# Optimization experiments

Hardware: AMD Instinct MI355X
Metric: run time of the kernel (lower is better)

## Reference

```python
import jax, jax.numpy as jnp
import numpy as np

B, TQ, TK = 2, 2048, 2048
D_IN, D_OUT, H = 1024, 1024, 16
HD = D_OUT // H  # head dim = 64


def setup_inputs() -> dict:
    key = jax.random.key(0)
    ks = jax.random.split(key, 11)
    s = 1.0 / np.sqrt(D_IN)
    so = 1.0 / np.sqrt(D_OUT)
    return {
        "q": jax.random.normal(ks[0], (B, TQ, D_IN), jnp.float32),
        "k": jax.random.normal(ks[1], (B, TK, D_IN), jnp.float32),
        "v": jax.random.normal(ks[2], (B, TK, D_IN), jnp.float32),
        "Wq": jax.random.uniform(ks[3], (D_OUT, D_IN), jnp.float32, -s, s),
        "bq": jax.random.uniform(ks[4], (D_OUT,), jnp.float32, -s, s),
        "Wk": jax.random.uniform(ks[5], (D_OUT, D_IN), jnp.float32, -s, s),
        "bk": jax.random.uniform(ks[6], (D_OUT,), jnp.float32, -s, s),
        "Wv": jax.random.uniform(ks[7], (D_OUT, D_IN), jnp.float32, -s, s),
        "bv": jax.random.uniform(ks[8], (D_OUT,), jnp.float32, -s, s),
        "Wo": jax.random.uniform(ks[9], (D_OUT, D_OUT), jnp.float32, -so, so),
        "bo": jax.random.uniform(ks[10], (D_OUT,), jnp.float32, -so, so),
    }


def reference(q, k, v, Wq, bq, Wk, bk, Wv, bv, Wo, bo):
    b, tq, _ = q.shape
    tk = k.shape[1]
    # linear projections, split heads: [B,T,D] -> [B,H,T,HD]
    qh = (q @ Wq.T + bq).reshape(b, tq, H, HD).transpose(0, 2, 1, 3)
    kh = (k @ Wk.T + bk).reshape(b, tk, H, HD).transpose(0, 2, 1, 3)
    vh = (v @ Wv.T + bv).reshape(b, tk, H, HD).transpose(0, 2, 1, 3)
    # scaled dot-product attention (forward never applies the causal mask)
    scores = jnp.einsum("bhqd,bhkd->bhqk", qh, kh) / np.sqrt(HD).astype(np.float32)
    attn = jax.nn.softmax(scores, axis=-1)
    x = jnp.einsum("bhqk,bhkd->bhqd", attn, vh)
    x = x.transpose(0, 2, 1, 3).reshape(b, tq, D_OUT)
    return x @ Wo.T + bo
```

## Files before the change

### kernel.cpp

```cpp
#include <hip/hip_runtime.h>
#include <hip/hip_bf16.h>

typedef __bf16 b16x8 __attribute__((ext_vector_type(8)));
typedef unsigned short u16x8 __attribute__((ext_vector_type(8)));
typedef unsigned short u16x4 __attribute__((ext_vector_type(4)));
typedef unsigned int u32x4 __attribute__((ext_vector_type(4)));
typedef unsigned int u32x2 __attribute__((ext_vector_type(2)));
typedef float f32x4 __attribute__((ext_vector_type(4)));
typedef float f32x16 __attribute__((ext_vector_type(16)));

__device__ __forceinline__ unsigned short f2b(float f) {
  unsigned u = __builtin_bit_cast(unsigned, f);
  u += 0x7fff + ((u >> 16) & 1);
  return (unsigned short)(u >> 16);
}

__device__ __forceinline__ b16x8 as_b(u16x8 v) { return __builtin_bit_cast(b16x8, v); }

__device__ __forceinline__ float fexp2(float x) {
#if __has_builtin(__builtin_amdgcn_exp2f)
  return __builtin_amdgcn_exp2f(x);
#else
  return exp2f(x);
#endif
}

__device__ __forceinline__ unsigned cvtpk(float lo, float hi) {
  unsigned r;
  asm("v_cvt_pk_bf16_f32 %0, %1, %2" : "=v"(r) : "v"(lo), "v"(hi));
  return r;
}

__device__ __forceinline__ void plswap(unsigned& a, unsigned& b) {
  asm volatile("v_permlane32_swap_b32 %0, %1" : "+v"(a), "+v"(b));
}

__device__ __forceinline__ b16x8 mkchunk(float p0, float p1, float p2, float p3,
                                         float p4, float p5, float p6, float p7) {
  unsigned a1 = cvtpk(p0, p1), b1 = cvtpk(p4, p5);
  unsigned a2 = cvtpk(p2, p3), b2 = cvtpk(p6, p7);
  plswap(a1, b1);
  plswap(a2, b2);
  u32x4 w = {a1, a2, b1, b2};
  return __builtin_bit_cast(b16x8, w);
}

#define AS1 __attribute__((address_space(1)))
#define AS3 __attribute__((address_space(3)))
__device__ __forceinline__ void gload_lds16(const void* g, void* l) {
  __builtin_amdgcn_global_load_lds((const AS1 void*)g, (AS3 void*)l, 16, 0, 0);
}

#define WAITV4() asm volatile("s_waitcnt vmcnt(4)" ::: "memory")
#define WAITV0() asm volatile("s_waitcnt vmcnt(0)" ::: "memory")
#define LGKM0()  asm volatile("s_waitcnt lgkmcnt(0)" ::: "memory")
#define BARRIER() asm volatile("s_barrier" ::: "memory")


__global__ __launch_bounds__(256) void convert_kernel(
    const float* __restrict__ q, const float* __restrict__ k, const float* __restrict__ v,
    const float* __restrict__ Wq, const float* __restrict__ Wk,
    const float* __restrict__ Wv, const float* __restrict__ Wo,
    unsigned short* __restrict__ qb, unsigned short* __restrict__ kb,
    unsigned short* __restrict__ vb, unsigned short* __restrict__ wqb,
    unsigned short* __restrict__ wkb, unsigned short* __restrict__ wvb,
    unsigned short* __restrict__ wob) {
  const float* src; unsigned short* dst; int rows;
  switch (blockIdx.y) {
    case 0: src = q;  dst = qb;  rows = 4096; break;
    case 1: src = k;  dst = kb;  rows = 4096; break;
    case 2: src = v;  dst = vb;  rows = 4096; break;
    case 3: src = Wq; dst = wqb; rows = 1024; break;
    case 4: src = Wk; dst = wkb; rows = 1024; break;
    case 5: src = Wv; dst = wvb; rows = 1024; break;
    default: src = Wo; dst = wob; rows = 1024; break;
  }
  const int row = blockIdx.x * 2 + (threadIdx.x >> 7);
  if (row >= rows) return;
  const int t = threadIdx.x & 127;
  const float* sp = src + (size_t)row * 1024 + t * 8;
  float4 f0 = *(const float4*)sp;
  float4 f1 = *(const float4*)(sp + 4);
  u16x8 h = { f2b(f0.x), f2b(f0.y), f2b(f0.z), f2b(f0.w),
              f2b(f1.x), f2b(f1.y), f2b(f1.z), f2b(f1.w) };
  const int swcol = ((t >> 3) << 6) | (((t & 7) ^ (row & 7)) << 3);
  *(u16x8*)(dst + (size_t)row * 1024 + swcol) = h;
}

template <int MODE, typename TOUT>
__device__ __forceinline__ void gemm_compute_step(const unsigned short* sA,
                                                  const unsigned short* sB,
                                                  f32x4 (&acc)[2][4],
                                                  int wm, int wn, int lr, int lg) {
  b16x8 af[2][2], bf[4][2];
#pragma unroll
  for (int mb = 0; mb < 2; ++mb)
#pragma unroll
    for (int kh = 0; kh < 2; ++kh) {
      const int r = wm * 32 + mb * 16 + lr;
      af[mb][kh] = as_b(*(const u16x8*)(&sA[(r * 64 + kh * 32 + lg * 8) ^ ((r & 7) << 3)]));
    }
#pragma unroll
  for (int nb = 0; nb < 4; ++nb)
#pragma unroll
    for (int kh = 0; kh < 2; ++kh) {
      const int r = wn * 64 + nb * 16 + lr;
      bf[nb][kh] = as_b(*(const u16x8*)(&sB[(r * 64 + kh * 32 + lg * 8) ^ ((r & 7) << 3)]));
    }
#pragma unroll
  for (int mb = 0; mb < 2; ++mb)
#pragma unroll
    for (int nb = 0; nb < 4; ++nb) {
      acc[mb][nb] = __builtin_amdgcn_mfma_f32_16x16x32_bf16(af[mb][0], bf[nb][0], acc[mb][nb], 0, 0, 0);
      acc[mb][nb] = __builtin_amdgcn_mfma_f32_16x16x32_bf16(af[mb][1], bf[nb][1], acc[mb][nb], 0, 0, 0);
    }
}

template <int MODE, typename TOUT>
__device__ __forceinline__ void gemm_epilogue(f32x4 (&acc)[2][4],
                                              const float* __restrict__ bias,
                                              TOUT* __restrict__ C,
                                              int bm, int bn, int wm, int wn,
                                              int lr, int lg) {
  const float qscale = 0.125f * 1.44269504f;
#pragma unroll
  for (int mb = 0; mb < 2; ++mb)
#pragma unroll
    for (int nb = 0; nb < 4; ++nb) {
      const int c = bn + wn * 64 + nb * 16 + lr;
      const float bv = bias[c];
      const int r0 = bm + wm * 32 + mb * 16 + lg * 4;
      if constexpr (MODE == 2) {
        const int hh = c >> 6, hd = c & 63;
        const int bb = r0 >> 11, t0 = r0 & 2047;
        u16x4 pk = { f2b(acc[mb][nb][0] + bv), f2b(acc[mb][nb][1] + bv),
                     f2b(acc[mb][nb][2] + bv), f2b(acc[mb][nb][3] + bv) };
        const int tsw = (t0 & ~63) | (((((t0 >> 3) & 7) ^ (hd & 7)) << 3)) | (t0 & 7);
        *(u16x4*)(&C[(((size_t)bb * 16 + hh) * 64 + hd) * 2048 + tsw]) = pk;
      } else {
#pragma unroll
        for (int i = 0; i < 4; ++i) {
          float val = acc[mb][nb][i] + bv;
          if constexpr (MODE == 1) val *= qscale;
          if constexpr (MODE == 3) {
            C[(size_t)(r0 + i) * 1024 + c] = val;
          } else {
            const int cc = (c & ~63) | (((((c >> 3) & 7) ^ ((r0 + i) & 7)) << 3)) | (c & 7);
            C[(size_t)(r0 + i) * 1024 + cc] = (TOUT)f2b(val);
          }
        }
      }
    }
}

template <int MODE, typename TOUT>
__device__ __forceinline__ void gemm_b16A(unsigned short* sA, unsigned short* sB,
                                          const unsigned short* __restrict__ A,
                                          const unsigned short* __restrict__ Bm,
                                          const float* __restrict__ bias,
                                          TOUT* __restrict__ C,
                                          int bm, int bn) {
  const int tid = threadIdx.x;
  const int l = tid & 63, w = tid >> 6;
  const int wm = w >> 1, wn = w & 1;
  const int lr = l & 15, lg = l >> 4;
  const int r8 = l >> 3, sl = l & 7;

  f32x4 acc[2][4] = {};

  for (int k0 = 0; k0 < 1024; k0 += 64) {
#pragma unroll
    for (int i = 0; i < 2; ++i) {
      gload_lds16(A + (size_t)(bm + i * 32 + w * 8 + r8) * 1024 + k0 + sl * 8,
                  &sA[i * 2048 + w * 512]);
    }
#pragma unroll
    for (int i = 0; i < 4; ++i) {
      const int row = i * 32 + w * 8 + r8;
      gload_lds16(Bm + (size_t)(bn + row) * 1024 + k0 + sl * 8, &sB[i * 2048 + w * 512]);
    }
    __syncthreads();
    gemm_compute_step<MODE, TOUT>(sA, sB, acc, wm, wn, lr, lg);
    __syncthreads();
  }
  gemm_epilogue<MODE, TOUT>(acc, bias, C, bm, bn, wm, wn, lr, lg);
}

__global__ __launch_bounds__(256) void proj_kernel(
    const unsigned short* __restrict__ qb, const unsigned short* __restrict__ kb,
    const unsigned short* __restrict__ vb,
    const unsigned short* __restrict__ wqb, const float* __restrict__ bq,
    const unsigned short* __restrict__ wkb, const float* __restrict__ bk,
    const unsigned short* __restrict__ wvb, const float* __restrict__ bv,
    unsigned short* __restrict__ Qh, unsigned short* __restrict__ Kh,
    unsigned short* __restrict__ Vt) {
  __shared__ __align__(16) unsigned short sA[64 * 64];
  __shared__ __align__(16) unsigned short sB[128 * 64];
  const int id = blockIdx.x;
  const int g = id >> 6, r = id & 63;
  const int bn = (r >> 3) * 128;
  const int panel = g * 8 + (r & 7);
  const int bz = panel >> 6;
  const int bm = (panel & 63) * 64;
  if (bz == 0)      gemm_b16A<1, unsigned short>(sA, sB, qb, wqb, bq, Qh, bm, bn);
  else if (bz == 1) gemm_b16A<0, unsigned short>(sA, sB, kb, wkb, bk, Kh, bm, bn);
  else              gemm_b16A<2, unsigned short>(sA, sB, vb, wvb, bv, Vt, bm, bn);
}

__global__ __launch_bounds__(256) void out_kernel(
    const unsigned short* __restrict__ X, const unsigned short* __restrict__ wob,
    const float* __restrict__ bo, float* __restrict__ out) {
  __shared__ __align__(16) unsigned short sA[64 * 64];
  __shared__ __align__(16) unsigned short sB[128 * 64];
  const int id = blockIdx.x;
  const int g = id >> 6, r = id & 63;
  const int bn = (r >> 3) * 128;
  const int bm = (g * 8 + (r & 7)) * 64;
  gemm_b16A<3, float>(sA, sB, X, wob, bo, out, bm, bn);
}

__global__ __launch_bounds__(512, 4) void attn_kernel(
    const unsigned short* __restrict__ Qh, const unsigned short* __restrict__ Kh,
    const unsigned short* __restrict__ Vt, unsigned short* __restrict__ X) {
  __shared__ __align__(16) unsigned short sMem[8][4096];

  const int tid = threadIdx.x;
  const int l = tid & 63, wq = tid >> 6;
  const int half = wq >> 2, w4 = wq & 3;
  const int lq = l & 31, lg = l >> 5;

  const int id = blockIdx.x + (int)(gridDim.x * blockIdx.y);
  const int id2 = (id & 7) * 64 + (id >> 3);
  const int bx = id2 & 15, by = id2 >> 4;
  const int b = by >> 4, h = by & 15;
  const int q0 = bx * 128 + w4 * 32;
  const int kvbase = half * 1024;

  const size_t baseQK = (size_t)b * 2048 * 1024 + (size_t)h * 64;
  const size_t baseV  = ((size_t)(b * 16 + h)) * 64 * 2048;

  unsigned short* sK0 = &sMem[half * 4 + 0][0];
  unsigned short* sK1 = &sMem[half * 4 + 1][0];
  unsigned short* sV0 = &sMem[half * 4 + 2][0];
  unsigned short* sV1 = &sMem[half * 4 + 3][0];

  const int rk = lq & 7;
  b16x8 qf0, qf1, qf2, qf3;
  {
    const unsigned short* qp = Qh + baseQK + (size_t)(q0 + lq) * 1024;
    qf0 = as_b(*(const u16x8*)(qp + (((0 + lg) ^ rk) << 3)));
    qf1 = as_b(*(const u16x8*)(qp + (((2 + lg) ^ rk) << 3)));
    qf2 = as_b(*(const u16x8*)(qp + (((4 + lg) ^ rk) << 3)));
    qf3 = as_b(*(const u16x8*)(qp + (((6 + lg) ^ rk) << 3)));
  }

  const int r8 = l >> 3, sl = l & 7;

  auto stageKV = [&](unsigned short* dK, unsigned short* dV, int kv0) {
#pragma unroll
    for (int i = 0; i < 2; ++i) {
      const int rowb = 16 * w4 + 8 * i;
      gload_lds16(Kh + baseQK + (size_t)(kv0 + rowb + r8) * 1024 + sl * 8, dK + rowb * 64);
      gload_lds16(Vt + baseV + (size_t)(rowb + r8) * 2048 + kv0 + sl * 8, dV + rowb * 64);
    }
  };

  float m_run = 0.f, l_run = 0.f;
  f32x16 Oa = {}, Ob = {};
  const int sw = (lq & 7) << 3;

  auto body = [&](const unsigned short* K_, const unsigned short* V_) {
    f32x16 s0, s1;
#pragma unroll
    for (int j = 0; j < 16; ++j) { s0[j] = -m_run; s1[j] = -m_run; }
    __builtin_amdgcn_s_setprio(1);
#pragma unroll
    for (int c = 0; c < 4; ++c) {
      const int hd8 = c * 16 + 8 * lg;
      b16x8 kf0 = as_b(*(const u16x8*)(&K_[lq * 64 + (hd8 ^ sw)]));
      b16x8 kf1 = as_b(*(const u16x8*)(&K_[(32 + lq) * 64 + (hd8 ^ sw)]));
      b16x8 qf = (c == 0) ? qf0 : (c == 1) ? qf1 : (c == 2) ? qf2 : qf3;
      s0 = __builtin_amdgcn_mfma_f32_32x32x16_bf16(kf0, qf, s0, 0, 0, 0);
      s1 = __builtin_amdgcn_mfma_f32_32x32x16_bf16(kf1, qf, s1, 0, 0, 0);
    }
    __builtin_amdgcn_s_setprio(0);

    float a0 = fmaxf(fmaxf(s0[0], s0[1]), fmaxf(s0[2], s0[3]));
    float a1 = fmaxf(fmaxf(s0[4], s0[5]), fmaxf(s0[6], s0[7]));
    float a2 = fmaxf(fmaxf(s0[8], s0[9]), fmaxf(s0[10], s0[11]));
    float a3 = fmaxf(fmaxf(s0[12], s0[13]), fmaxf(s0[14], s0[15]));
    float a4 = fmaxf(fmaxf(s1[0], s1[1]), fmaxf(s1[2], s1[3]));
    float a5 = fmaxf(fmaxf(s1[4], s1[5]), fmaxf(s1[6], s1[7]));
    float a6 = fmaxf(fmaxf(s1[8], s1[9]), fmaxf(s1[10], s1[11]));
    float a7 = fmaxf(fmaxf(s1[12], s1[13]), fmaxf(s1[14], s1[15]));
    float mx = fmaxf(fmaxf(fmaxf(a0, a1), fmaxf(a2, a3)),
                     fmaxf(fmaxf(a4, a5), fmaxf(a6, a7)));
    mx = fmaxf(mx, __shfl_xor(mx, 32));

    if (__any(mx > 8.0f)) {
      const float dm = fmaxf(mx, 0.f);
      const float al = fexp2(-dm);
      m_run += dm;
      l_run *= al;
#pragma unroll
      for (int j = 0; j < 16; ++j) {
        Oa[j] *= al; Ob[j] *= al; s0[j] -= dm; s1[j] -= dm;
      }
    }

#pragma unroll
    for (int j = 0; j < 16; ++j) s0[j] = fexp2(s0[j]);
#pragma unroll
    for (int j = 0; j < 16; ++j) s1[j] = fexp2(s1[j]);

    float r0 = ((s0[0] + s0[1]) + (s0[2] + s0[3])) + ((s0[4] + s0[5]) + (s0[6] + s0[7]));
    float r1 = ((s0[8] + s0[9]) + (s0[10] + s0[11])) + ((s0[12] + s0[13]) + (s0[14] + s0[15]));
    float r2 = ((s1[0] + s1[1]) + (s1[2] + s1[3])) + ((s1[4] + s1[5]) + (s1[6] + s1[7]));
    float r3 = ((s1[8] + s1[9]) + (s1[10] + s1[11])) + ((s1[12] + s1[13]) + (s1[14] + s1[15]));
    float rs = (r0 + r1) + (r2 + r3);
    rs += __shfl_xor(rs, 32);
    l_run += rs;

    b16x8 pb0 = mkchunk(s0[0], s0[1], s0[2], s0[3], s0[4], s0[5], s0[6], s0[7]);
    b16x8 pb1 = mkchunk(s0[8], s0[9], s0[10], s0[11], s0[12], s0[13], s0[14], s0[15]);
    b16x8 pb2 = mkchunk(s1[0], s1[1], s1[2], s1[3], s1[4], s1[5], s1[6], s1[7]);
    b16x8 pb3 = mkchunk(s1[8], s1[9], s1[10], s1[11], s1[12], s1[13], s1[14], s1[15]);

    __builtin_amdgcn_s_setprio(1);
#pragma unroll
    for (int c = 0; c < 4; ++c) {
      const int kv8 = c * 16 + 8 * lg;
      b16x8 vfa = as_b(*(const u16x8*)(&V_[lq * 64 + (kv8 ^ sw)]));
      b16x8 vfb = as_b(*(const u16x8*)(&V_[(32 + lq) * 64 + (kv8 ^ sw)]));
      b16x8 pb = (c == 0) ? pb0 : (c == 1) ? pb1 : (c == 2) ? pb2 : pb3;
      Oa = __builtin_amdgcn_mfma_f32_32x32x16_bf16(vfa, pb, Oa, 0, 0, 0);
      Ob = __builtin_amdgcn_mfma_f32_32x32x16_bf16(vfb, pb, Ob, 0, 0, 0);
    }
    __builtin_amdgcn_s_setprio(0);
  };

  stageKV(sK0, sV0, kvbase);
  stageKV(sK1, sV1, kvbase + 64);

#pragma unroll 1
  for (int tt = 0; tt < 16; tt += 2) {
    WAITV4();
    BARRIER();
    body(sK0, sV0);
    LGKM0();
    BARRIER();
    if (tt + 2 < 16) stageKV(sK0, sV0, kvbase + (tt + 2) * 64);

    if (tt + 3 < 16) { WAITV4(); } else { WAITV0(); }
    BARRIER();
    body(sK1, sV1);
    LGKM0();
    BARRIER();
    if (tt + 3 < 16) stageKV(sK1, sV1, kvbase + (tt + 3) * 64);
  }

  float* fb = (float*)&sMem[0][0];
  const int mbase = w4 * 64 + l;
  if (half == 1) {
    fb[0 * 256 + mbase] = m_run;
    fb[1 * 256 + mbase] = l_run;
#pragma unroll
    for (int j = 0; j < 16; ++j) fb[(2 + j) * 256 + mbase] = Oa[j];
#pragma unroll
    for (int j = 0; j < 16; ++j) fb[(18 + j) * 256 + mbase] = Ob[j];
  }
  __syncthreads();
  if (half == 0) {
    const float m2 = fb[0 * 256 + mbase], l2 = fb[1 * 256 + mbase];
    const float mM = fmaxf(m_run, m2);
    const float c1 = fexp2(m_run - mM), c2 = fexp2(m2 - mM);
    const float inv = 1.0f / (l_run * c1 + l2 * c2);
    const float ia = c1 * inv, ib = c2 * inv;
#pragma unroll
    for (int j = 0; j < 16; ++j) {
      Oa[j] = Oa[j] * ia + fb[(2 + j) * 256 + mbase] * ib;
      Ob[j] = Ob[j] * ia + fb[(18 + j) * 256 + mbase] * ib;
    }
    unsigned short* xp = X + baseQK + (size_t)(q0 + lq) * 1024;
#pragma unroll
    for (int g = 0; g < 4; ++g) {
      u32x2 wa = { cvtpk(Oa[4 * g + 0], Oa[4 * g + 1]),
                   cvtpk(Oa[4 * g + 2], Oa[4 * g + 3]) };
      *(u32x2*)(xp + ((g ^ rk) << 3) + 4 * lg) = wa;
      u32x2 wb = { cvtpk(Ob[4 * g + 0], Ob[4 * g + 1]),
                   cvtpk(Ob[4 * g + 2], Ob[4 * g + 3]) };
      *(u32x2*)(xp + (((4 + g) ^ rk) << 3) + 4 * lg) = wb;
    }
  }
}

extern "C" void kernel_launch(void* const* d_in, const int* in_sizes, int n_in,
                              void* d_out, int out_size, void* d_ws, size_t ws_size,
                              hipStream_t stream) {
  const float* q  = (const float*)d_in[0];
  const float* k  = (const float*)d_in[1];
  const float* v  = (const float*)d_in[2];
  const float* Wq = (const float*)d_in[3];
  const float* bq = (const float*)d_in[4];
  const float* Wk = (const float*)d_in[5];
  const float* bk = (const float*)d_in[6];
  const float* Wv = (const float*)d_in[7];
  const float* bv = (const float*)d_in[8];
  const float* Wo = (const float*)d_in[9];
  const float* bo = (const float*)d_in[10];

  unsigned short* ws = (unsigned short*)d_ws;
  const size_t M1 = (size_t)1024 * 1024;
  unsigned short* qb  = ws;
  unsigned short* kb  = ws + 4 * M1;
  unsigned short* vb  = ws + 8 * M1;
  unsigned short* wqb = ws + 12 * M1;
  unsigned short* wkb = ws + 13 * M1;
  unsigned short* wvb = ws + 14 * M1;
  unsigned short* wob = ws + 15 * M1;
  unsigned short* Qh  = ws + 16 * M1;
  unsigned short* Kh  = ws + 20 * M1;
  unsigned short* Vt  = ws + 24 * M1;
  unsigned short* X   = qb;

  dim3 blk(256);
  convert_kernel<<<dim3(2048, 7), blk, 0, stream>>>(q, k, v, Wq, Wk, Wv, Wo,
                                                    qb, kb, vb, wqb, wkb, wvb, wob);
  proj_kernel<<<dim3(1536), blk, 0, stream>>>(qb, kb, vb, wqb, bq, wkb, bk, wvb, bv,
                                              Qh, Kh, Vt);
  attn_kernel<<<dim3(16, 32), dim3(512), 0, stream>>>(Qh, Kh, Vt, X);
  out_kernel<<<dim3(512), blk, 0, stream>>>(X, wob, bo, (float*)d_out);
}
```

Before: 117.9 us.

## Single-buffer attention K/V tiles to halve LDS and raise occupancy

The attention kernel drops its double-buffered K/V staging in favour of a single LDS buffer per half, so each iteration loads, waits for all loads, computes and then synchronises. LDS use shrinks and launch bounds go from 4 to 8 blocks per CU, aiming to hide memory latency through more resident waves rather than software prefetch. The GEMM compute step is also inlined directly into the loop. The cost is no overlap of the next tile's loads with the current tile's compute inside a block, plus a tighter register budget that could cause spills.

```diff
diff --git a/kernel.cpp b/kernel.cpp
--- a/kernel.cpp
+++ b/kernel.cpp
@@ -51,9 +51,7 @@
   __builtin_amdgcn_global_load_lds((const AS1 void*)g, (AS3 void*)l, 16, 0, 0);
 }
 
-#define WAITV4() asm volatile("s_waitcnt vmcnt(4)" ::: "memory")
 #define WAITV0() asm volatile("s_waitcnt vmcnt(0)" ::: "memory")
-#define LGKM0()  asm volatile("s_waitcnt lgkmcnt(0)" ::: "memory")
 #define BARRIER() asm volatile("s_barrier" ::: "memory")
 
 
@@ -88,35 +86,6 @@
 }
 
 template <int MODE, typename TOUT>
-__device__ __forceinline__ void gemm_compute_step(const unsigned short* sA,
-                                                  const unsigned short* sB,
-                                                  f32x4 (&acc)[2][4],
-                                                  int wm, int wn, int lr, int lg) {
-  b16x8 af[2][2], bf[4][2];
-#pragma unroll
-  for (int mb = 0; mb < 2; ++mb)
-#pragma unroll
-    for (int kh = 0; kh < 2; ++kh) {
-      const int r = wm * 32 + mb * 16 + lr;
-      af[mb][kh] = as_b(*(const u16x8*)(&sA[(r * 64 + kh * 32 + lg * 8) ^ ((r & 7) << 3)]));
-    }
-#pragma unroll
-  for (int nb = 0; nb < 4; ++nb)
-#pragma unroll
-    for (int kh = 0; kh < 2; ++kh) {
-      const int r = wn * 64 + nb * 16 + lr;
-      bf[nb][kh] = as_b(*(const u16x8*)(&sB[(r * 64 + kh * 32 + lg * 8) ^ ((r & 7) << 3)]));
-    }
-#pragma unroll
-  for (int mb = 0; mb < 2; ++mb)
-#pragma unroll
-    for (int nb = 0; nb < 4; ++nb) {
-      acc[mb][nb] = __builtin_amdgcn_mfma_f32_16x16x32_bf16(af[mb][0], bf[nb][0], acc[mb][nb], 0, 0, 0);
-      acc[mb][nb] = __builtin_amdgcn_mfma_f32_16x16x32_bf16(af[mb][1], bf[nb][1], acc[mb][nb], 0, 0, 0);
-    }
-}
-
-template <int MODE, typename TOUT>
 __device__ __forceinline__ void gemm_epilogue(f32x4 (&acc)[2][4],
                                               const float* __restrict__ bias,
                                               TOUT* __restrict__ C,
@@ -180,7 +149,29 @@
       gload_lds16(Bm + (size_t)(bn + row) * 1024 + k0 + sl * 8, &sB[i * 2048 + w * 512]);
     }
     __syncthreads();
-    gemm_compute_step<MODE, TOUT>(sA, sB, acc, wm, wn, lr, lg);
+
+    b16x8 af[2][2], bf[4][2];
+#pragma unroll
+    for (int mb = 0; mb < 2; ++mb)
+#pragma unroll
+      for (int kh = 0; kh < 2; ++kh) {
+        const int r = wm * 32 + mb * 16 + lr;
+        af[mb][kh] = as_b(*(const u16x8*)(&sA[(r * 64 + kh * 32 + lg * 8) ^ ((r & 7) << 3)]));
+      }
+#pragma unroll
+    for (int nb = 0; nb < 4; ++nb)
+#pragma unroll
+      for (int kh = 0; kh < 2; ++kh) {
+        const int r = wn * 64 + nb * 16 + lr;
+        bf[nb][kh] = as_b(*(const u16x8*)(&sB[(r * 64 + kh * 32 + lg * 8) ^ ((r & 7) << 3)]));
+      }
+#pragma unroll
+    for (int mb = 0; mb < 2; ++mb)
+#pragma unroll
+      for (int nb = 0; nb < 4; ++nb) {
+        acc[mb][nb] = __builtin_amdgcn_mfma_f32_16x16x32_bf16(af[mb][0], bf[nb][0], acc[mb][nb], 0, 0, 0);
+        acc[mb][nb] = __builtin_amdgcn_mfma_f32_16x16x32_bf16(af[mb][1], bf[nb][1], acc[mb][nb], 0, 0, 0);
+      }
     __syncthreads();
   }
   gemm_epilogue<MODE, TOUT>(acc, bias, C, bm, bn, wm, wn, lr, lg);
@@ -219,10 +210,10 @@
   gemm_b16A<3, float>(sA, sB, X, wob, bo, out, bm, bn);
 }
 
-__global__ __launch_bounds__(512, 4) void attn_kernel(
+__global__ __launch_bounds__(512, 8) void attn_kernel(
     const unsigned short* __restrict__ Qh, const unsigned short* __restrict__ Kh,
     const unsigned short* __restrict__ Vt, unsigned short* __restrict__ X) {
-  __shared__ __align__(16) unsigned short sMem[8][4096];
+  __shared__ __align__(16) unsigned short sMem[17408];
 
   const int tid = threadIdx.x;
   const int l = tid & 63, wq = tid >> 6;
@@ -239,10 +230,8 @@
   const size_t baseQK = (size_t)b * 2048 * 1024 + (size_t)h * 64;
   const size_t baseV  = ((size_t)(b * 16 + h)) * 64 * 2048;
 
-  unsigned short* sK0 = &sMem[half * 4 + 0][0];
-  unsigned short* sK1 = &sMem[half * 4 + 1][0];
-  unsigned short* sV0 = &sMem[half * 4 + 2][0];
-  unsigned short* sV1 = &sMem[half * 4 + 3][0];
+  unsigned short* sK = &sMem[half * 8192];
+  unsigned short* sV = &sMem[half * 8192 + 4096];
 
   const int rk = lq & 7;
   b16x8 qf0, qf1, qf2, qf3;
@@ -256,12 +245,12 @@
 
   const int r8 = l >> 3, sl = l & 7;
 
-  auto stageKV = [&](unsigned short* dK, unsigned short* dV, int kv0) {
+  auto stageKV = [&](int kv0) {
 #pragma unroll
     for (int i = 0; i < 2; ++i) {
       const int rowb = 16 * w4 + 8 * i;
-      gload_lds16(Kh + baseQK + (size_t)(kv0 + rowb + r8) * 1024 + sl * 8, dK + rowb * 64);
-      gload_lds16(Vt + baseV + (size_t)(rowb + r8) * 2048 + kv0 + sl * 8, dV + rowb * 64);
+      gload_lds16(Kh + baseQK + (size_t)(kv0 + rowb + r8) * 1024 + sl * 8, sK + rowb * 64);
+      gload_lds16(Vt + baseV + (size_t)(rowb + r8) * 2048 + kv0 + sl * 8, sV + rowb * 64);
     }
   };
 
@@ -269,7 +258,9 @@
   f32x16 Oa = {}, Ob = {};
   const int sw = (lq & 7) << 3;
 
-  auto body = [&](const unsigned short* K_, const unsigned short* V_) {
+  auto body = [&]() {
+    const unsigned short* K_ = sK;
+    const unsigned short* V_ = sV;
     f32x16 s0, s1;
 #pragma unroll
     for (int j = 0; j < 16; ++j) { s0[j] = -m_run; s1[j] = -m_run; }
@@ -339,27 +330,16 @@
     __builtin_amdgcn_s_setprio(0);
   };
 
-  stageKV(sK0, sV0, kvbase);
-  stageKV(sK1, sV1, kvbase + 64);
-
 #pragma unroll 1
-  for (int tt = 0; tt < 16; tt += 2) {
-    WAITV4();
+  for (int t = 0; t < 16; ++t) {
+    stageKV(kvbase + t * 64);
+    WAITV0();
     BARRIER();
-    body(sK0, sV0);
-    LGKM0();
+    body();
     BARRIER();
-    if (tt + 2 < 16) stageKV(sK0, sV0, kvbase + (tt + 2) * 64);
-
-    if (tt + 3 < 16) { WAITV4(); } else { WAITV0(); }
-    BARRIER();
-    body(sK1, sV1);
-    LGKM0();
-    BARRIER();
-    if (tt + 3 < 16) stageKV(sK1, sV1, kvbase + (tt + 3) * 64);
-  }
-
-  float* fb = (float*)&sMem[0][0];
+  }
+
+  float* fb = (float*)&sMem[0];
   const int mbase = w4 * 64 + l;
   if (half == 1) {
     fb[0 * 256 + mbase] = m_run;
```

Result: slower. 427.5 us (+262.4%).
